# Optimization experiments

Measured on AMD Instinct MI355X. Metric: run time of the kernel, lower is better.

## Reference

```python
import jax, jax.numpy as jnp
import numpy as np
import math

LEVEL_SHAPES = [(100, 152), (50, 76), (25, 38), (13, 19)]
BS, E, NH, NL, NP = 2, 256, 8, 4, 4


def _grid_init_bias(num_heads, num_levels, num_points):
    # faithful to MultiScaleDeformableAttention.init_weights sampling_offsets bias
    thetas = jnp.arange(num_heads, dtype=jnp.float32) * (2.0 * math.pi / num_heads)
    grid = jnp.stack([jnp.cos(thetas), jnp.sin(thetas)], -1)  # [H,2]
    grid = grid / jnp.max(jnp.abs(grid), axis=-1, keepdims=True)
    grid = jnp.tile(grid[:, None, None, :], (1, num_levels, num_points, 1))  # [H,L,P,2]
    scale = jnp.arange(1, num_points + 1, dtype=jnp.float32)[None, None, :, None]
    return (grid * scale).reshape(-1)


def setup_inputs() -> dict:
    key = jax.random.key(0)
    ks = jax.random.split(key, 10)
    nv = sum(h * w for h, w in LEVEL_SHAPES)  # 20197
    nq = nv
    query = jax.random.normal(ks[0], (BS, nq, E), dtype=jnp.float32)
    value = jax.random.normal(ks[1], (BS, nv, E), dtype=jnp.float32)
    reference_points = jax.random.uniform(ks[2], (BS, nq, NL, 2), dtype=jnp.float32)
    spatial_shapes = jnp.array(LEVEL_SHAPES, dtype=jnp.int32)
    sizes = [h * w for h, w in LEVEL_SHAPES]
    level_start_index = jnp.array(np.cumsum([0] + sizes)[:-1], dtype=jnp.int32)
    s = 1.0 / math.sqrt(E)
    # Linear params stored as [in, out]; y = x @ W + b
    Wv = jax.random.normal(ks[3], (E, E), dtype=jnp.float32) * s
    bv = jnp.zeros((E,), jnp.float32)
    Wso = jax.random.normal(ks[4], (E, NH * NL * NP * 2), dtype=jnp.float32) * 0.01
    bso = _grid_init_bias(NH, NL, NP)
    Waw = jax.random.normal(ks[5], (E, NH * NL * NP), dtype=jnp.float32) * 0.01
    baw = jnp.zeros((NH * NL * NP,), jnp.float32)
    Wo = jax.random.normal(ks[6], (E, E), dtype=jnp.float32) * s
    bo = jnp.zeros((E,), jnp.float32)
    return dict(query=query, value=value, reference_points=reference_points,
                spatial_shapes=spatial_shapes, level_start_index=level_start_index,
                Wv=Wv, bv=bv, Wso=Wso, bso=bso, Waw=Waw, baw=baw, Wo=Wo, bo=bo)


def _bilinear_sample(vl, loc, h, w):
    # vl: [bs, nh, h*w, d]; loc: [bs, nq, nh, P, 2] normalized in [0,1]
    # matches F.grid_sample(mode='bilinear', padding_mode='zeros', align_corners=False)
    bs, nh, _, d = vl.shape
    nq, P = loc.shape[1], loc.shape[3]
    x = loc[..., 0] * w - 0.5
    y = loc[..., 1] * h - 0.5
    x0 = jnp.floor(x).astype(jnp.int32); x1 = x0 + 1
    y0 = jnp.floor(y).astype(jnp.int32); y1 = y0 + 1
    wx1 = x - x0; wx0 = 1.0 - wx1
    wy1 = y - y0; wy0 = 1.0 - wy1

    def gather(ix, iy):
        valid = ((ix >= 0) & (ix < w) & (iy >= 0) & (iy < h)).astype(vl.dtype)
        idx = jnp.clip(iy, 0, h - 1) * w + jnp.clip(ix, 0, w - 1)  # [bs,nq,nh,P]
        idx = jnp.transpose(idx, (0, 2, 1, 3)).reshape(bs, nh, nq * P)
        g = jnp.take_along_axis(vl, idx[..., None], axis=2)  # [bs,nh,nq*P,d]
        g = g.reshape(bs, nh, nq, P, d).transpose(0, 2, 1, 3, 4)  # [bs,nq,nh,P,d]
        return g * valid[..., None]

    return (gather(x0, y0) * (wx0 * wy0)[..., None]
            + gather(x1, y0) * (wx1 * wy0)[..., None]
            + gather(x0, y1) * (wx0 * wy1)[..., None]
            + gather(x1, y1) * (wx1 * wy1)[..., None])


def reference(query, value, reference_points, spatial_shapes, level_start_index,
              Wv, bv, Wso, bso, Waw, baw, Wo, bo):
    bs, nq, e = query.shape
    nv = value.shape[1]
    nh, nl, npt = NH, NL, NP
    d = e // nh
    shapes = np.asarray(spatial_shapes)          # static level shapes
    starts = np.asarray(level_start_index)

    v = (value @ Wv + bv).reshape(bs, nv, nh, d).transpose(0, 2, 1, 3)  # [bs,nh,nv,d]
    so = (query @ Wso + bso).reshape(bs, nq, nh, nl, npt, 2)
    aw = jax.nn.softmax((query @ Waw + baw).reshape(bs, nq, nh, nl * npt), axis=-1)
    aw = aw.reshape(bs, nq, nh, nl, npt)

    # offset normalizer is (w, h) per level
    offset_norm = jnp.stack([spatial_shapes[:, 1], spatial_shapes[:, 0]], -1).astype(query.dtype)
    loc = reference_points[:, :, None, :, None, :] + so / offset_norm[None, None, None, :, None, :]

    out = jnp.zeros((bs, nq, nh, d), dtype=query.dtype)
    for l in range(nl):
        h, w = int(shapes[l, 0]), int(shapes[l, 1])
        s = int(starts[l])
        vl = v[:, :, s:s + h * w, :]                      # [bs,nh,h*w,d]
        sampled = _bilinear_sample(vl, loc[:, :, :, l], h, w)  # [bs,nq,nh,P,d]
        out = out + jnp.einsum('bqhpd,bqhp->bqhd', sampled, aw[:, :, :, l])

    out = out.reshape(bs, nq, e) @ Wo + bo
    return out + query  # identity residual (dropout in eval mode)
```

## Files before the change

### kernel.cpp

```cpp
#include <hip/hip_runtime.h>
#include <hip/hip_bf16.h>
#include <math.h>

constexpr int kBS = 2;
constexpr int kNQ = 20197;
constexpr int kNV = 20197;
constexpr int kM  = kBS * kNQ;
constexpr int kMT = 632;
constexpr int kMpad = kMT * 64;

__constant__ int cLH[4] = {100, 50, 25, 13};
__constant__ int cLW[4] = {152, 76, 38, 19};
__constant__ int cLS[4] = {0, 15200, 19000, 19950};

typedef __bf16 bf16x8 __attribute__((ext_vector_type(8)));
typedef float  f32x4  __attribute__((ext_vector_type(4)));

__device__ __forceinline__ unsigned short f2bf(float x) {
    unsigned u = __float_as_uint(x);
    return (unsigned short)((u + 0x7fffu + ((u >> 16) & 1u)) >> 16);
}
__device__ __forceinline__ unsigned pack2(float a, float b) {
    return (unsigned)f2bf(a) | ((unsigned)f2bf(b) << 16);
}
__device__ __forceinline__ float bflo(unsigned u) { return __uint_as_float(u << 16); }
__device__ __forceinline__ float bfhi(unsigned u) { return __uint_as_float(u & 0xffff0000u); }
__device__ __forceinline__ void gload_lds16(const void* g, void* s) {
    __builtin_amdgcn_global_load_lds(
        (const __attribute__((address_space(1))) void*)g,
        (__attribute__((address_space(3))) void*)s, 16, 0, 0);
}

__global__ __launch_bounds__(256) void prep_w(
    const float* __restrict__ Wv, const float* __restrict__ Wso,
    const float* __restrict__ Waw, const float* __restrict__ Wo,
    const float* __restrict__ bso, const float* __restrict__ baw,
    unsigned short* __restrict__ WvT, unsigned short* __restrict__ WsoawT,
    unsigned short* __restrict__ WoT, float* __restrict__ bias384)
{
    int k = blockIdx.x * 256 + threadIdx.x;
    if (k < 65536) { WvT[k] = f2bf(Wv[(k & 255) * 256 + (k >> 8)]); return; }
    k -= 65536;
    if (k < 98304) {
        int n = k >> 8, kk = k & 255;
        WsoawT[k] = f2bf(n < 256 ? Wso[kk * 256 + n] : Waw[kk * 128 + (n - 256)]);
        return;
    }
    k -= 98304;
    if (k < 65536) { WoT[k] = f2bf(Wo[(k & 255) * 256 + (k >> 8)]); return; }
    k -= 65536;
    if (k < 384) bias384[k] = (k < 256) ? bso[k] : baw[k - 256];
}

template<int AFP32, int CFP32>
__device__ __forceinline__ void gemm_core(
    const void* __restrict__ Av, const __hip_bfloat16* __restrict__ BT,
    const float* __restrict__ bias, const float* __restrict__ res,
    int N, int NT, void* __restrict__ Cv, int m0)
{
    __shared__ __hip_bfloat16 As[64 * 264];
    __shared__ __hip_bfloat16 Bs[2][128 * 32];

    const int t = threadIdx.x;
    const int wave = t >> 6, lane = t & 63;
    const int quad = lane >> 4, l16 = lane & 15;
    const int mw = (wave & 1) * 32, nw = (wave >> 1) * 64;

    auto issueB = [&](int nti, int kc, int buf) {
        #pragma unroll
        for (int j = 0; j < 2; ++j) {
            int off = j * 4096 + t * 16;
            int row = off >> 6, kb = off & 63;
            gload_lds16((const char*)BT + (size_t)(nti * 128 + row) * 512 + kc * 64 + kb,
                        (char*)&Bs[buf][0] + off);
        }
    };

    issueB(0, 0, 0);

    if (AFP32) {
        const float* af = (const float*)Av;
        #pragma unroll
        for (int p = 0; p < 16; ++p) {
            int idx = p * 256 + t;
            int row = idx >> 6, col4 = idx & 63;
            float4 f = make_float4(0.f, 0.f, 0.f, 0.f);
            if (m0 + row < kM)
                f = *(const float4*)(af + (size_t)(m0 + row) * 256 + col4 * 4);
            uint2 u = make_uint2(pack2(f.x, f.y), pack2(f.z, f.w));
            *(uint2*)(void*)&As[row * 264 + col4 * 4] = u;
        }
    } else {
        const unsigned short* ab = (const unsigned short*)Av;
        #pragma unroll
        for (int p = 0; p < 8; ++p) {
            int idx = p * 256 + t;
            int row = idx >> 5, ch = idx & 31;
            uint4 u = *(const uint4*)(ab + (size_t)(m0 + row) * 256 + ch * 8);
            *(uint4*)(void*)&As[row * 264 + ch * 8] = u;
        }
    }

    for (int nti = 0; nti < NT; ++nti) {
        f32x4 acc[2][4] = {};
        for (int kc = 0; kc < 8; ++kc) {
            __syncthreads();
            if (kc < 7)             issueB(nti, kc + 1, (kc + 1) & 1);
            else if (nti + 1 < NT)  issueB(nti + 1, 0, 0);
            bf16x8 afr[2], bfr[4];
            #pragma unroll
            for (int mt = 0; mt < 2; ++mt)
                afr[mt] = *(const bf16x8*)(const void*)
                    &As[(mw + mt * 16 + l16) * 264 + kc * 32 + quad * 8];
            #pragma unroll
            for (int nt = 0; nt < 4; ++nt)
                bfr[nt] = *(const bf16x8*)(const void*)
                    &Bs[kc & 1][(nw + nt * 16 + l16) * 32 + quad * 8];
            #pragma unroll
            for (int mt = 0; mt < 2; ++mt)
                #pragma unroll
                for (int nt = 0; nt < 4; ++nt)
                    acc[mt][nt] = __builtin_amdgcn_mfma_f32_16x16x32_bf16(
                        afr[mt], bfr[nt], acc[mt][nt], 0, 0, 0);
        }
        const int n0g = nti * 128;
        #pragma unroll
        for (int nt = 0; nt < 4; ++nt) {
            int col = n0g + nw + nt * 16 + l16;
            float bvv = bias[col];
            #pragma unroll
            for (int mt = 0; mt < 2; ++mt) {
                #pragma unroll
                for (int i = 0; i < 4; ++i) {
                    int row = m0 + mw + mt * 16 + quad * 4 + i;
                    if (row < kM) {
                        float val = acc[mt][nt][i] + bvv;
                        if (CFP32)
                            ((float*)Cv)[(size_t)row * N + col] =
                                val + res[(size_t)row * N + col];
                        else
                            ((unsigned short*)Cv)[(size_t)row * N + col] = f2bf(val);
                    }
                }
            }
        }
    }
}

__global__ __launch_bounds__(256, 3) void gemm_dual(
    const float* __restrict__ value, const __hip_bfloat16* __restrict__ WvT,
    const float* __restrict__ bv, unsigned short* __restrict__ v_b,
    const float* __restrict__ query, const __hip_bfloat16* __restrict__ WsoawT,
    const float* __restrict__ b384, unsigned short* __restrict__ soaw)
{
    const int m0 = blockIdx.y * 64;
    const float* A; const __hip_bfloat16* BT; const float* bias;
    unsigned short* C; int N, NT;
    if (blockIdx.x == 0) { A = value; BT = WvT;    bias = bv;   C = v_b;  N = 256; NT = 2; }
    else                 { A = query; BT = WsoawT; bias = b384; C = soaw; N = 384; NT = 3; }
    gemm_core<1, 0>(A, BT, bias, nullptr, N, NT, C, m0);
}

__global__ __launch_bounds__(256, 3) void gemm_final(
    const unsigned short* __restrict__ mid_b, const __hip_bfloat16* __restrict__ WoT,
    const float* __restrict__ bo, const float* __restrict__ query,
    float* __restrict__ out)
{
    gemm_core<0, 1>(mid_b, WoT, bo, query, 256, 2, out, blockIdx.y * 64);
}

__global__ __launch_bounds__(128) void msda_sample(
    const __hip_bfloat16* __restrict__ v,
    const __hip_bfloat16* __restrict__ soaw,
    const float* __restrict__ rp,
    __hip_bfloat16* __restrict__ mid)
{
    const int bq = blockIdx.x;
    const int b  = bq >= kNQ;
    const int t  = threadIdx.x;

    __shared__ int   sOff[128 * 5];
    __shared__ float sW[128 * 5];

    {
        const int h = t >> 4, lp = t & 15, l = lp >> 2;
        unsigned sopk = *(const unsigned*)(const void*)(soaw + (size_t)bq * 384 + 2 * t);
        float logit = bflo((unsigned)*(const unsigned short*)(const void*)
                           (soaw + (size_t)bq * 384 + 256 + t));
        float2 rr = *(const float2*)(rp + (size_t)bq * 8 + l * 2);
        float sx = bflo(sopk), sy = bfhi(sopk);

        float mx = logit;
        #pragma unroll
        for (int s = 8; s >= 1; s >>= 1) mx = fmaxf(mx, __shfl_xor(mx, s, 16));
        float e = __expf(logit - mx);
        float sum = e;
        #pragma unroll
        for (int s = 8; s >= 1; s >>= 1) sum += __shfl_xor(sum, s, 16);
        float w = e / sum;

        const int ww = cLW[l], hh = cLH[l];
        const float fw = (float)ww, fh = (float)hh;
        float x = rr.x * fw + sx - 0.5f;
        float y = rr.y * fh + sy - 0.5f;
        float xf = floorf(x), yf = floorf(y);
        int x0 = (int)xf, y0 = (int)yf;
        float wx1 = x - xf, wx0 = 1.f - wx1;
        float wy1 = y - yf, wy0 = 1.f - wy1;
        bool vx0 = (x0 >= 0) & (x0 < ww);
        bool vx1 = (x0 >= -1) & (x0 + 1 < ww);
        bool vy0 = (y0 >= 0) & (y0 < hh);
        bool vy1 = (y0 >= -1) & (y0 + 1 < hh);
        int cx0 = min(max(x0, 0), ww - 1);
        int cx1 = min(max(x0 + 1, 0), ww - 1);
        int cy0 = min(max(y0, 0), hh - 1);
        int cy1 = min(max(y0 + 1, 0), hh - 1);
        const int base = cLS[l] * 256 + h * 32;
        sOff[t * 5 + 0] = base + (cy0 * ww + cx0) * 256;
        sOff[t * 5 + 1] = base + (cy0 * ww + cx1) * 256;
        sOff[t * 5 + 2] = base + (cy1 * ww + cx0) * 256;
        sOff[t * 5 + 3] = base + (cy1 * ww + cx1) * 256;
        sW[t * 5 + 0] = (vx0 & vy0) ? w * wx0 * wy0 : 0.f;
        sW[t * 5 + 1] = (vx1 & vy0) ? w * wx1 * wy0 : 0.f;
        sW[t * 5 + 2] = (vx0 & vy1) ? w * wx0 * wy1 : 0.f;
        sW[t * 5 + 3] = (vx1 & vy1) ? w * wx1 * wy1 : 0.f;
    }
    __syncthreads();

    const int h = t >> 4, c = (t & 15) * 2;
    const __hip_bfloat16* vb = v + (size_t)b * kNV * 256 + c;
    float accx = 0.f, accy = 0.f;
    const int p0 = h * 16;
    #pragma unroll 4
    for (int pp = 0; pp < 16; ++pp) {
        const int idx = (p0 + pp) * 5;
        #pragma unroll
        for (int k2 = 0; k2 < 4; ++k2) {
            float wgt = sW[idx + k2];
            int   off = sOff[idx + k2];
            unsigned u = *(const unsigned*)(const void*)(vb + off);
            accx += wgt * bflo(u);
            accy += wgt * bfhi(u);
        }
    }
    *(unsigned*)(void*)(mid + (size_t)bq * 256 + h * 32 + c) = pack2(accx, accy);
}

extern "C" void kernel_launch(void* const* d_in, const int* in_sizes, int n_in,
                              void* d_out, int out_size, void* d_ws, size_t ws_size,
                              hipStream_t stream)
{
    const float* query = (const float*)d_in[0];
    const float* value = (const float*)d_in[1];
    const float* rp    = (const float*)d_in[2];
    const float* Wv  = (const float*)d_in[5];
    const float* bv  = (const float*)d_in[6];
    const float* Wso = (const float*)d_in[7];
    const float* bso = (const float*)d_in[8];
    const float* Waw = (const float*)d_in[9];
    const float* baw = (const float*)d_in[10];
    const float* Wo  = (const float*)d_in[11];
    const float* bo  = (const float*)d_in[12];

    unsigned short* v_b = (unsigned short*)d_out;

    char* p = (char*)d_ws;
    __hip_bfloat16* soaw  = (__hip_bfloat16*)p;  p += (size_t)kM * 384 * 2;
    unsigned short* mid_b = (unsigned short*)p;  p += (size_t)kMpad * 256 * 2;
    unsigned short* WvT    = (unsigned short*)p; p += 256 * 256 * 2;
    unsigned short* WsoawT = (unsigned short*)p; p += 384 * 256 * 2;
    unsigned short* WoT    = (unsigned short*)p; p += 256 * 256 * 2;
    float* bias384         = (float*)p;

    hipLaunchKernelGGL(prep_w, dim3(898), dim3(256), 0, stream,
                       Wv, Wso, Waw, Wo, bso, baw, WvT, WsoawT, WoT, bias384);

    hipLaunchKernelGGL(gemm_dual, dim3(2, kMT), dim3(256), 0, stream,
                       value, (const __hip_bfloat16*)WvT, bv, v_b,
                       query, (const __hip_bfloat16*)WsoawT, bias384,
                       (unsigned short*)soaw);

    hipLaunchKernelGGL(msda_sample, dim3(kM), dim3(128), 0, stream,
                       (const __hip_bfloat16*)v_b, soaw, rp, (__hip_bfloat16*)mid_b);

    hipLaunchKernelGGL(gemm_final, dim3(1, kMT), dim3(256), 0, stream,
                       mid_b, (const __hip_bfloat16*)WoT, bo, query, (float*)d_out);
}
```

Before: 299.6 us.

## Keep weight fragments in registers and stream A rows directly in GEMMs

Both GEMM kernels drop shared-memory tiling. Each wave now holds its 64-column slice of the bf16 weight matrix in registers for the whole K=256 and streams 16-row A fragments straight from global memory into MFMA. The grid becomes a flat persistent-style layout: 474 blocks of 256 rows for the projection GEMMs and 316 blocks of 128 rows for the output GEMM. The aim is to remove LDS traffic and barriers, at the cost of heavy register use (launch bounds drop to 2 blocks per CU) and uncoalesced per-lane row loads of A.

```diff
diff --git a/kernel.cpp b/kernel.cpp
--- a/kernel.cpp
+++ b/kernel.cpp
@@ -6,8 +6,7 @@
 constexpr int kNQ = 20197;
 constexpr int kNV = 20197;
 constexpr int kM  = kBS * kNQ;
-constexpr int kMT = 632;
-constexpr int kMpad = kMT * 64;
+constexpr int kMpad = 40448;
 
 __constant__ int cLH[4] = {100, 50, 25, 13};
 __constant__ int cLW[4] = {152, 76, 38, 19};
@@ -15,6 +14,7 @@
 
 typedef __bf16 bf16x8 __attribute__((ext_vector_type(8)));
 typedef float  f32x4  __attribute__((ext_vector_type(4)));
+typedef unsigned uintx4 __attribute__((ext_vector_type(4)));
 
 __device__ __forceinline__ unsigned short f2bf(float x) {
     unsigned u = __float_as_uint(x);
@@ -25,11 +25,6 @@
 }
 __device__ __forceinline__ float bflo(unsigned u) { return __uint_as_float(u << 16); }
 __device__ __forceinline__ float bfhi(unsigned u) { return __uint_as_float(u & 0xffff0000u); }
-__device__ __forceinline__ void gload_lds16(const void* g, void* s) {
-    __builtin_amdgcn_global_load_lds(
-        (const __attribute__((address_space(1))) void*)g,
-        (__attribute__((address_space(3))) void*)s, 16, 0, 0);
-}
 
 __global__ __launch_bounds__(256) void prep_w(
     const float* __restrict__ Wv, const float* __restrict__ Wso,
@@ -52,121 +47,113 @@
     if (k < 384) bias384[k] = (k < 256) ? bso[k] : baw[k - 256];
 }
 
-template<int AFP32, int CFP32>
-__device__ __forceinline__ void gemm_core(
-    const void* __restrict__ Av, const __hip_bfloat16* __restrict__ BT,
-    const float* __restrict__ bias, const float* __restrict__ res,
-    int N, int NT, void* __restrict__ Cv, int m0)
-{
-    __shared__ __hip_bfloat16 As[64 * 264];
-    __shared__ __hip_bfloat16 Bs[2][128 * 32];
-
-    const int t = threadIdx.x;
-    const int wave = t >> 6, lane = t & 63;
-    const int quad = lane >> 4, l16 = lane & 15;
-    const int mw = (wave & 1) * 32, nw = (wave >> 1) * 64;
-
-    auto issueB = [&](int nti, int kc, int buf) {
-        #pragma unroll
-        for (int j = 0; j < 2; ++j) {
-            int off = j * 4096 + t * 16;
-            int row = off >> 6, kb = off & 63;
-            gload_lds16((const char*)BT + (size_t)(nti * 128 + row) * 512 + kc * 64 + kb,
-                        (char*)&Bs[buf][0] + off);
-        }
-    };
-
-    issueB(0, 0, 0);
-
-    if (AFP32) {
-        const float* af = (const float*)Av;
-        #pragma unroll
-        for (int p = 0; p < 16; ++p) {
-            int idx = p * 256 + t;
-            int row = idx >> 6, col4 = idx & 63;
-            float4 f = make_float4(0.f, 0.f, 0.f, 0.f);
-            if (m0 + row < kM)
-                f = *(const float4*)(af + (size_t)(m0 + row) * 256 + col4 * 4);
-            uint2 u = make_uint2(pack2(f.x, f.y), pack2(f.z, f.w));
-            *(uint2*)(void*)&As[row * 264 + col4 * 4] = u;
-        }
-    } else {
-        const unsigned short* ab = (const unsigned short*)Av;
-        #pragma unroll
-        for (int p = 0; p < 8; ++p) {
-            int idx = p * 256 + t;
-            int row = idx >> 5, ch = idx & 31;
-            uint4 u = *(const uint4*)(ab + (size_t)(m0 + row) * 256 + ch * 8);
-            *(uint4*)(void*)&As[row * 264 + ch * 8] = u;
-        }
-    }
-
-    for (int nti = 0; nti < NT; ++nti) {
-        f32x4 acc[2][4] = {};
+__global__ __launch_bounds__(256, 2) void gemm_fused(
+    const float* __restrict__ value, const float* __restrict__ query,
+    const __hip_bfloat16* __restrict__ WvT, const __hip_bfloat16* __restrict__ WsoawT,
+    const float* __restrict__ bv, const float* __restrict__ b384,
+    unsigned short* __restrict__ v_b, unsigned short* __restrict__ soaw)
+{
+    const int bx = blockIdx.x, t = threadIdx.x;
+    const int wave = t >> 6, lane = t & 63, quad = lane >> 4, l16 = lane & 15;
+
+    const float* A; const __hip_bfloat16* BT; const float* bias; unsigned short* C;
+    int N, n0w, mstart, ntiles;
+    if (bx < 158)      { A = value; BT = WvT;    bias = bv;   C = v_b;  N = 256;
+                         n0w = wave * 64; mstart = bx * 256; ntiles = 16; }
+    else if (bx < 316) { A = query; BT = WsoawT; bias = b384; C = soaw; N = 384;
+                         n0w = wave * 64; mstart = (bx - 158) * 256; ntiles = 16; }
+    else               { A = query; BT = WsoawT; bias = b384; C = soaw; N = 384;
+                         n0w = 256 + (wave & 1) * 64;
+                         mstart = (bx - 316) * 256 + (wave >> 1) * 128; ntiles = 8; }
+
+    bf16x8 Bf[4][8];
+    #pragma unroll
+    for (int nt = 0; nt < 4; ++nt)
+        #pragma unroll
+        for (int kc = 0; kc < 8; ++kc)
+            Bf[nt][kc] = *(const bf16x8*)(const void*)
+                (BT + (size_t)(n0w + nt * 16 + l16) * 256 + kc * 32 + quad * 8);
+
+    for (int it = 0; it < ntiles; ++it) {
+        const int m0 = mstart + it * 16;
+        const int arow = min(m0 + l16, kM - 1);
+        const float* ap = A + (size_t)arow * 256 + quad * 8;
+        float4 a0[8], a1[8];
+        #pragma unroll
         for (int kc = 0; kc < 8; ++kc) {
-            __syncthreads();
-            if (kc < 7)             issueB(nti, kc + 1, (kc + 1) & 1);
-            else if (nti + 1 < NT)  issueB(nti + 1, 0, 0);
-            bf16x8 afr[2], bfr[4];
-            #pragma unroll
-            for (int mt = 0; mt < 2; ++mt)
-                afr[mt] = *(const bf16x8*)(const void*)
-                    &As[(mw + mt * 16 + l16) * 264 + kc * 32 + quad * 8];
+            a0[kc] = *(const float4*)(ap + kc * 32);
+            a1[kc] = *(const float4*)(ap + kc * 32 + 4);
+        }
+        f32x4 acc[4] = {};
+        #pragma unroll
+        for (int kc = 0; kc < 8; ++kc) {
+            uintx4 u = { pack2(a0[kc].x, a0[kc].y), pack2(a0[kc].z, a0[kc].w),
+                         pack2(a1[kc].x, a1[kc].y), pack2(a1[kc].z, a1[kc].w) };
+            bf16x8 af = __builtin_bit_cast(bf16x8, u);
             #pragma unroll
             for (int nt = 0; nt < 4; ++nt)
-                bfr[nt] = *(const bf16x8*)(const void*)
-                    &Bs[kc & 1][(nw + nt * 16 + l16) * 32 + quad * 8];
-            #pragma unroll
-            for (int mt = 0; mt < 2; ++mt)
-                #pragma unroll
-                for (int nt = 0; nt < 4; ++nt)
-                    acc[mt][nt] = __builtin_amdgcn_mfma_f32_16x16x32_bf16(
-                        afr[mt], bfr[nt], acc[mt][nt], 0, 0, 0);
-        }
-        const int n0g = nti * 128;
+                acc[nt] = __builtin_amdgcn_mfma_f32_16x16x32_bf16(
+                    af, Bf[nt][kc], acc[nt], 0, 0, 0);
+        }
         #pragma unroll
         for (int nt = 0; nt < 4; ++nt) {
-            int col = n0g + nw + nt * 16 + l16;
-            float bvv = bias[col];
-            #pragma unroll
-            for (int mt = 0; mt < 2; ++mt) {
-                #pragma unroll
-                for (int i = 0; i < 4; ++i) {
-                    int row = m0 + mw + mt * 16 + quad * 4 + i;
-                    if (row < kM) {
-                        float val = acc[mt][nt][i] + bvv;
-                        if (CFP32)
-                            ((float*)Cv)[(size_t)row * N + col] =
-                                val + res[(size_t)row * N + col];
-                        else
-                            ((unsigned short*)Cv)[(size_t)row * N + col] = f2bf(val);
-                    }
-                }
+            const int col = n0w + nt * 16 + l16;
+            const float bvv = bias[col];
+            #pragma unroll
+            for (int i = 0; i < 4; ++i) {
+                const int row = m0 + quad * 4 + i;
+                if (row < kM)
+                    C[(size_t)row * N + col] = f2bf(acc[nt][i] + bvv);
             }
         }
     }
 }
 
-__global__ __launch_bounds__(256, 3) void gemm_dual(
-    const float* __restrict__ value, const __hip_bfloat16* __restrict__ WvT,
-    const float* __restrict__ bv, unsigned short* __restrict__ v_b,
-    const float* __restrict__ query, const __hip_bfloat16* __restrict__ WsoawT,
-    const float* __restrict__ b384, unsigned short* __restrict__ soaw)
-{
-    const int m0 = blockIdx.y * 64;
-    const float* A; const __hip_bfloat16* BT; const float* bias;
-    unsigned short* C; int N, NT;
-    if (blockIdx.x == 0) { A = value; BT = WvT;    bias = bv;   C = v_b;  N = 256; NT = 2; }
-    else                 { A = query; BT = WsoawT; bias = b384; C = soaw; N = 384; NT = 3; }
-    gemm_core<1, 0>(A, BT, bias, nullptr, N, NT, C, m0);
-}
-
-__global__ __launch_bounds__(256, 3) void gemm_final(
+__global__ __launch_bounds__(256, 2) void gemm_final(
     const unsigned short* __restrict__ mid_b, const __hip_bfloat16* __restrict__ WoT,
     const float* __restrict__ bo, const float* __restrict__ query,
     float* __restrict__ out)
 {
-    gemm_core<0, 1>(mid_b, WoT, bo, query, 256, 2, out, blockIdx.y * 64);
+    const int bx = blockIdx.x, t = threadIdx.x;
+    const int wave = t >> 6, lane = t & 63, quad = lane >> 4, l16 = lane & 15;
+    const int n0w = wave * 64, mstart = bx * 128;
+
+    bf16x8 Bf[4][8];
+    #pragma unroll
+    for (int nt = 0; nt < 4; ++nt)
+        #pragma unroll
+        for (int kc = 0; kc < 8; ++kc)
+            Bf[nt][kc] = *(const bf16x8*)(const void*)
+                (WoT + (size_t)(n0w + nt * 16 + l16) * 256 + kc * 32 + quad * 8);
+
+    for (int it = 0; it < 8; ++it) {
+        const int m0 = mstart + it * 16;
+        const __hip_bfloat16* ap =
+            (const __hip_bfloat16*)mid_b + (size_t)(m0 + l16) * 256 + quad * 8;
+        bf16x8 af[8];
+        #pragma unroll
+        for (int kc = 0; kc < 8; ++kc)
+            af[kc] = *(const bf16x8*)(const void*)(ap + kc * 32);
+        f32x4 acc[4] = {};
+        #pragma unroll
+        for (int kc = 0; kc < 8; ++kc)
+            #pragma unroll
+            for (int nt = 0; nt < 4; ++nt)
+                acc[nt] = __builtin_amdgcn_mfma_f32_16x16x32_bf16(
+                    af[kc], Bf[nt][kc], acc[nt], 0, 0, 0);
+        #pragma unroll
+        for (int nt = 0; nt < 4; ++nt) {
+            const int col = n0w + nt * 16 + l16;
+            const float bvv = bo[col];
+            #pragma unroll
+            for (int i = 0; i < 4; ++i) {
+                const int row = m0 + quad * 4 + i;
+                if (row < kM)
+                    out[(size_t)row * 256 + col] =
+                        acc[nt][i] + bvv + query[(size_t)row * 256 + col];
+            }
+        }
+    }
 }
 
 __global__ __launch_bounds__(128) void msda_sample(
@@ -275,14 +262,14 @@
     hipLaunchKernelGGL(prep_w, dim3(898), dim3(256), 0, stream,
                        Wv, Wso, Waw, Wo, bso, baw, WvT, WsoawT, WoT, bias384);
 
-    hipLaunchKernelGGL(gemm_dual, dim3(2, kMT), dim3(256), 0, stream,
-                       value, (const __hip_bfloat16*)WvT, bv, v_b,
-                       query, (const __hip_bfloat16*)WsoawT, bias384,
-                       (unsigned short*)soaw);
+    hipLaunchKernelGGL(gemm_fused, dim3(474), dim3(256), 0, stream,
+                       value, query, (const __hip_bfloat16*)WvT,
+                       (const __hip_bfloat16*)WsoawT, bv, bias384,
+                       v_b, (unsigned short*)soaw);
 
     hipLaunchKernelGGL(msda_sample, dim3(kM), dim3(128), 0, stream,
                        (const __hip_bfloat16*)v_b, soaw, rp, (__hip_bfloat16*)mid_b);
 
-    hipLaunchKernelGGL(gemm_final, dim3(1, kMT), dim3(256), 0, stream,
+    hipLaunchKernelGGL(gemm_final, dim3(316), dim3(256), 0, stream,
                        mid_b, (const __hip_bfloat16*)WoT, bo, query, (float*)d_out);
 }
```

Measured after the change: 357.5 us. 19.3% more time.
